# Optimization experiments

Hardware: AMD Instinct MI355X
Metric: run time of the kernel (lower is better)

Reference implementation:

```python
import jax, jax.numpy as jnp
import numpy as np

DIM = 256
HEADS = 4
B, N = 2, 4096
NEG = -1e9
EPS = 1e-5


def setup_inputs() -> dict:
    key = jax.random.key(0)
    ks = jax.random.split(key, 12)
    s = 0.02
    inp = {
        "x": jax.random.normal(ks[0], (B, N, DIM), dtype=jnp.float32),
        "adj": jax.random.randint(ks[1], (B, N, N), 0, 2, dtype=jnp.int32),
        "Wq": jax.random.normal(ks[2], (DIM, DIM), dtype=jnp.float32) * s,
        "bq": jnp.zeros((DIM,), jnp.float32),
        "Wk": jax.random.normal(ks[3], (DIM, DIM), dtype=jnp.float32) * s,
        "bk": jnp.zeros((DIM,), jnp.float32),
        "Wv": jax.random.normal(ks[4], (DIM, DIM), dtype=jnp.float32) * s,
        "bv": jnp.zeros((DIM,), jnp.float32),
        "Wo": jax.random.normal(ks[5], (DIM, DIM), dtype=jnp.float32) * s,
        "bo": jnp.zeros((DIM,), jnp.float32),
        "gamma": jnp.ones((DIM,), jnp.float32),
        "beta": jnp.zeros((DIM,), jnp.float32),
    }
    return inp


def reference(x, adj, Wq, bq, Wk, bk, Wv, bv, Wo, bo, gamma, beta):
    Bx, Nx, C = x.shape
    H = HEADS
    D = C // H
    scale = D ** (-0.5)
    # torch Linear: y = x @ W.T + b
    def proj(W, b):
        return (x @ W.T + b).reshape(Bx, Nx, H, D).transpose(0, 2, 1, 3)  # [B,H,N,D]
    q = proj(Wq, bq)
    k = proj(Wk, bk)
    v = proj(Wv, bv)
    attn = jnp.einsum("bhnd,bhmd->bhnm", q, k) * scale          # [B,H,N,N]
    attn = jnp.where(adj[:, None, :, :] == 0, NEG, attn)
    attn = jax.nn.softmax(attn, axis=-1)
    # dropout omitted (eval mode / deterministic reference)
    out = jnp.einsum("bhnm,bhmd->bhnd", attn, v)                # [B,H,N,D]
    out = out.transpose(0, 2, 1, 3).reshape(Bx, Nx, C)
    out = out @ Wo.T + bo
    mu = jnp.mean(out, axis=-1, keepdims=True)
    var = jnp.var(out, axis=-1, keepdims=True)
    return (out - mu) * jax.lax.rsqrt(var + EPS) * gamma + beta
```

## Files before the change

### kernel.cpp

```cpp
#include <hip/hip_runtime.h>
#include <stdint.h>

#define CDIM 256
#define HEADS 4
#define HD 64
#define NB 2
#define NN 4096

typedef unsigned short u16;
typedef unsigned char u8;
typedef unsigned long long u64;
typedef __attribute__((ext_vector_type(8))) short short8;
typedef __attribute__((ext_vector_type(4))) float f32x4;
typedef __attribute__((ext_vector_type(16))) float f32x16;

#define QSCALE 0.1803368801111244f

__device__ __forceinline__ u16 f2bf(float f) {
  union { float f; unsigned u; } v; v.f = f;
  return (u16)((v.u + 0x7fffu + ((v.u >> 16) & 1u)) >> 16);
}
__device__ __forceinline__ float bf2f(u16 u) {
  union { unsigned u; float f; } v; v.u = ((unsigned)u) << 16; return v.f;
}
__device__ __forceinline__ short8 fragf32(const float* p) {
  float4 a = reinterpret_cast<const float4*>(p)[0];
  float4 b = reinterpret_cast<const float4*>(p)[1];
  short8 h;
  h[0] = (short)f2bf(a.x); h[1] = (short)f2bf(a.y);
  h[2] = (short)f2bf(a.z); h[3] = (short)f2bf(a.w);
  h[4] = (short)f2bf(b.x); h[5] = (short)f2bf(b.y);
  h[6] = (short)f2bf(b.z); h[7] = (short)f2bf(b.w);
  return h;
}
__device__ __forceinline__ f32x16 zero16() {
  f32x16 z;
#pragma unroll
  for (int i = 0; i < 16; ++i) z[i] = 0.f;
  return z;
}
__device__ __forceinline__ unsigned cvt_pk_bf16(float lo, float hi) {
  unsigned r;
  asm("v_cvt_pk_bf16_f32 %0, %1, %2" : "=v"(r) : "v"(lo), "v"(hi));
  return r;
}
__device__ __forceinline__ void permlane32_swap(unsigned& a, unsigned& b) {
  asm("v_permlane32_swap_b32 %0, %1" : "+v"(a), "+v"(b));
}

__global__ __launch_bounds__(256) void prep(
    const int* __restrict__ adj, u8* __restrict__ bmb,
    const float* __restrict__ Wq, const float* __restrict__ Wk,
    const float* __restrict__ Wv, const float* __restrict__ Wo,
    u16* __restrict__ Wqb, u16* __restrict__ Wkb,
    u16* __restrict__ Wvb, u16* __restrict__ Wob) {
  const int blk = blockIdx.x;
  if (blk < 4096) {
    const int wave = threadIdx.x >> 6, lane = threadIdx.x & 63;
    const int c0 = blk * 16 + wave * 4;
#pragma unroll
    for (int it = 0; it < 4; ++it) {
      int c = c0 + it;
      int row = c >> 3, kb = (c & 7) * 512;
      const int* src = adj + (size_t)row * 4096 + kb + lane * 8;
      uint4 a = *reinterpret_cast<const uint4*>(src);
      uint4 b = *reinterpret_cast<const uint4*>(src + 4);
      unsigned byte = 0;
      byte |= (a.x != 0) ? 1u : 0u;
      byte |= (a.y != 0) ? 2u : 0u;
      byte |= (a.z != 0) ? 4u : 0u;
      byte |= (a.w != 0) ? 8u : 0u;
      byte |= (b.x != 0) ? 16u : 0u;
      byte |= (b.y != 0) ? 32u : 0u;
      byte |= (b.z != 0) ? 64u : 0u;
      byte |= (b.w != 0) ? 128u : 0u;
      bmb[(size_t)row * 512 + (c & 7) * 64 + lane] = (u8)byte;
    }
  } else {
    size_t base = ((size_t)(blk - 4096) * 256 + threadIdx.x) * 8;
    int w = (int)(base >> 16);
    size_t lo = base & 65535;
    const float* src;
    u16* dst;
    if (w == 0)      { src = Wq + lo; dst = Wqb + lo; }
    else if (w == 1) { src = Wk + lo; dst = Wkb + lo; }
    else if (w == 2) { src = Wv + lo; dst = Wvb + lo; }
    else             { src = Wo + lo; dst = Wob + lo; }
    *reinterpret_cast<short8*>(dst) = fragf32(src);
  }
}

__global__ __launch_bounds__(256) void qkv_gemm(
    const float* __restrict__ x,
    const u16* __restrict__ Wqb, const u16* __restrict__ Wkb,
    const u16* __restrict__ Wvb,
    const float* __restrict__ bq, const float* __restrict__ bk,
    const float* __restrict__ bv,
    u16* __restrict__ Qb, u16* __restrict__ Kb, u16* __restrict__ Vtb) {
  const int tid = threadIdx.x, w = tid >> 6, lane = tid & 63;
  const int quad = lane >> 4, l15 = lane & 15;
  const int tok0 = blockIdx.x * 16;
  const int b = tok0 >> 12, nl = tok0 & 4095;
  const int ym = blockIdx.y;

  f32x4 acc[4];
#pragma unroll
  for (int i = 0; i < 4; ++i) acc[i] = (f32x4){0.f, 0.f, 0.f, 0.f};

  if (ym < 2) {
    const u16* Wb = (ym == 0) ? Wqb : Wkb;
    const float* bias = (ym == 0) ? bq : bk;
    const float scale = (ym == 0) ? QSCALE : 1.0f;
    u16* outp = (ym == 0) ? Qb : Kb;
#pragma unroll
    for (int ks = 0; ks < 8; ++ks) {
      short8 af = fragf32(x + (size_t)(tok0 + l15) * 256 + ks * 32 + quad * 8);
#pragma unroll
      for (int ns = 0; ns < 4; ++ns) {
        short8 bf = *reinterpret_cast<const short8*>(
            &Wb[(size_t)(w * 64 + ns * 16 + l15) * 256 + ks * 32 + quad * 8]);
        acc[ns] = __builtin_amdgcn_mfma_f32_16x16x32_bf16(af, bf, acc[ns], 0, 0, 0);
      }
    }
#pragma unroll
    for (int ns = 0; ns < 4; ++ns) {
      int d = ns * 16 + l15;
      float bb = bias[w * 64 + d];
#pragma unroll
      for (int r = 0; r < 4; ++r) {
        int tok = nl + quad * 4 + r;
        outp[((size_t)(b * HEADS + w) * NN + tok) * HD + d] =
            f2bf((acc[ns][r] + bb) * scale);
      }
    }
  } else {
#pragma unroll
    for (int ks = 0; ks < 8; ++ks) {
      short8 xf = fragf32(x + (size_t)(tok0 + l15) * 256 + ks * 32 + quad * 8);
#pragma unroll
      for (int ms = 0; ms < 4; ++ms) {
        short8 wf = *reinterpret_cast<const short8*>(
            &Wvb[(size_t)(w * 64 + ms * 16 + l15) * 256 + ks * 32 + quad * 8]);
        acc[ms] = __builtin_amdgcn_mfma_f32_16x16x32_bf16(wf, xf, acc[ms], 0, 0, 0);
      }
    }
#pragma unroll
    for (int ms = 0; ms < 4; ++ms) {
#pragma unroll
      for (int r = 0; r < 4; ++r) {
        int d = ms * 16 + quad * 4 + r;
        float bb = bv[w * 64 + d];
        Vtb[((size_t)((b * HEADS + w) * HD + d)) * NN + nl + l15] =
            f2bf(acc[ms][r] + bb);
      }
    }
  }
}

__global__ __launch_bounds__(256, 3) void attn_mfma(
    const u16* __restrict__ Qb, const u16* __restrict__ Kb,
    const u16* __restrict__ Vtb, const u64* __restrict__ bm,
    u16* __restrict__ Opb, float* __restrict__ Lp) {
  __shared__ __align__(16) u16 KVs[2 * 8192];

  const int tid = threadIdx.x;
  const int wave = tid >> 6, lane = tid & 63;
  const int h5 = lane >> 5, l31 = lane & 31, l7 = lane & 7;
  const int bh = blockIdx.y, b = bh >> 2, h = bh & 3;
  const int q0 = blockIdx.x * 128 + wave * 32;
  const int quarter = blockIdx.z;
  const int key0 = quarter * 1024;
  const int NT = 16;

  const u16* qr = Qb + ((size_t)bh * NN + q0 + l31) * HD + h5 * 8;
  const short8 qf0 = *reinterpret_cast<const short8*>(qr);
  const short8 qf1 = *reinterpret_cast<const short8*>(qr + 16);
  const short8 qf2 = *reinterpret_cast<const short8*>(qr + 32);
  const short8 qf3 = *reinterpret_cast<const short8*>(qr + 48);

  short8 ones;
#pragma unroll
  for (int i = 0; i < 8; ++i) ones[i] = (short)0x3F80;

  f32x16 Oacc0 = zero16(), Oacc1 = zero16(), Oli = zero16();

  int sdk[4];
#pragma unroll
  for (int j = 0; j < 4; ++j) sdk[j] = ((2 * j + h5) ^ l7) << 3;

  const int srow = tid >> 2;
  const int wbu0 = ((((tid & 3) * 2)     ^ (srow & 7)) << 3) + srow * 64;
  const int wbu1 = ((((tid & 3) * 2 + 1) ^ (srow & 7)) << 3) + srow * 64;

  const u16* kbase = Kb + (size_t)bh * NN * HD + (size_t)key0 * HD;
  const u16* vbase = Vtb + (size_t)bh * HD * NN + key0;
  const u64* bmr = bm + ((size_t)b * NN + q0 + l31) * 64 + quarter * 16;

  uint4 k0, k1, v0, v1;
  {
    const uint4* kp = reinterpret_cast<const uint4*>(kbase) + tid * 2;
    k0 = kp[0]; k1 = kp[1];
    const u16* vp = vbase + (size_t)srow * NN + (tid & 3) * 16;
    v0 = *reinterpret_cast<const uint4*>(vp);
    v1 = *reinterpret_cast<const uint4*>(vp + 8);
  }
  *reinterpret_cast<uint4*>(&KVs[wbu0]) = k0;
  *reinterpret_cast<uint4*>(&KVs[wbu1]) = k1;
  *reinterpret_cast<uint4*>(&KVs[4096 + wbu0]) = v0;
  *reinterpret_cast<uint4*>(&KVs[4096 + wbu1]) = v1;
  {
    const uint4* kp = reinterpret_cast<const uint4*>(kbase + 4096) + tid * 2;
    k0 = kp[0]; k1 = kp[1];
    const u16* vp = vbase + (size_t)srow * NN + 64 + (tid & 3) * 16;
    v0 = *reinterpret_cast<const uint4*>(vp);
    v1 = *reinterpret_cast<const uint4*>(vp + 8);
  }
  u64 amc = bmr[0];

  for (int mt = 0; mt < NT; ++mt) {
    __syncthreads();
    const u64 am = amc;
    if (mt + 1 < NT) amc = bmr[mt + 1];
    const int cb = (mt & 1) * 8192;

    f32x16 s0 = zero16(), s1 = zero16();
    __builtin_amdgcn_s_setprio(1);
#pragma unroll
    for (int dk = 0; dk < 4; ++dk) {
      short8 a0 = *reinterpret_cast<const short8*>(&KVs[cb + l31 * 64 + sdk[dk]]);
      short8 a1 = *reinterpret_cast<const short8*>(&KVs[cb + 2048 + l31 * 64 + sdk[dk]]);
      const short8 qf = (dk == 0) ? qf0 : (dk == 1) ? qf1 : (dk == 2) ? qf2 : qf3;
      s0 = __builtin_amdgcn_mfma_f32_32x32x16_bf16(a0, qf, s0, 0, 0, 0);
      s1 = __builtin_amdgcn_mfma_f32_32x32x16_bf16(a1, qf, s1, 0, 0, 0);
    }
    __builtin_amdgcn_s_setprio(0);

    const u64 ash = am >> (4 * h5);
    const unsigned mlo = (unsigned)ash, mhi = (unsigned)(ash >> 32);

    uint4 pf0, pf1, pf2, pf3;
    {
      float pp[16];
#pragma unroll
      for (int r = 0; r < 16; ++r) {
        const int c = (r & 3) + 8 * (r >> 2);
        pp[r] = ((mlo >> c) & 1u) ? __builtin_amdgcn_exp2f(s0[r]) : 0.f;
      }
      unsigned wAe = cvt_pk_bf16(pp[0], pp[1]),  wBe = cvt_pk_bf16(pp[2], pp[3]);
      unsigned wAo = cvt_pk_bf16(pp[4], pp[5]),  wBo = cvt_pk_bf16(pp[6], pp[7]);
      permlane32_swap(wAe, wAo);
      permlane32_swap(wBe, wBo);
      pf0 = (uint4){wAe, wBe, wAo, wBo};
      wAe = cvt_pk_bf16(pp[8], pp[9]);   wBe = cvt_pk_bf16(pp[10], pp[11]);
      wAo = cvt_pk_bf16(pp[12], pp[13]); wBo = cvt_pk_bf16(pp[14], pp[15]);
      permlane32_swap(wAe, wAo);
      permlane32_swap(wBe, wBo);
      pf1 = (uint4){wAe, wBe, wAo, wBo};
    }
    {
      float pp[16];
#pragma unroll
      for (int r = 0; r < 16; ++r) {
        const int c = (r & 3) + 8 * (r >> 2);
        pp[r] = ((mhi >> c) & 1u) ? __builtin_amdgcn_exp2f(s1[r]) : 0.f;
      }
      unsigned wAe = cvt_pk_bf16(pp[0], pp[1]),  wBe = cvt_pk_bf16(pp[2], pp[3]);
      unsigned wAo = cvt_pk_bf16(pp[4], pp[5]),  wBo = cvt_pk_bf16(pp[6], pp[7]);
      permlane32_swap(wAe, wAo);
      permlane32_swap(wBe, wBo);
      pf2 = (uint4){wAe, wBe, wAo, wBo};
      wAe = cvt_pk_bf16(pp[8], pp[9]);   wBe = cvt_pk_bf16(pp[10], pp[11]);
      wAo = cvt_pk_bf16(pp[12], pp[13]); wBo = cvt_pk_bf16(pp[14], pp[15]);
      permlane32_swap(wAe, wAo);
      permlane32_swap(wBe, wBo);
      pf3 = (uint4){wAe, wBe, wAo, wBo};
    }

    __builtin_amdgcn_s_setprio(1);
#pragma unroll
    for (int kb = 0; kb < 4; ++kb) {
      union { uint4 u; short8 s; } cv;
      cv.u = (kb == 0) ? pf0 : (kb == 1) ? pf1 : (kb == 2) ? pf2 : pf3;
      const short8 pa = cv.s;
      Oli = __builtin_amdgcn_mfma_f32_32x32x16_bf16(pa, ones, Oli, 0, 0, 0);
      short8 vf0 = *reinterpret_cast<const short8*>(&KVs[cb + 4096 + l31 * 64 + sdk[kb]]);
      short8 vf1 = *reinterpret_cast<const short8*>(&KVs[cb + 6144 + l31 * 64 + sdk[kb]]);
      Oacc0 = __builtin_amdgcn_mfma_f32_32x32x16_bf16(pa, vf0, Oacc0, 0, 0, 0);
      Oacc1 = __builtin_amdgcn_mfma_f32_32x32x16_bf16(pa, vf1, Oacc1, 0, 0, 0);
    }
    __builtin_amdgcn_s_setprio(0);

    if (mt + 1 < NT) {
      const int nb = ((mt + 1) & 1) * 8192;
      *reinterpret_cast<uint4*>(&KVs[nb + wbu0]) = k0;
      *reinterpret_cast<uint4*>(&KVs[nb + wbu1]) = k1;
      *reinterpret_cast<uint4*>(&KVs[nb + 4096 + wbu0]) = v0;
      *reinterpret_cast<uint4*>(&KVs[nb + 4096 + wbu1]) = v1;
      if (mt + 2 < NT) {
        const uint4* kp =
            reinterpret_cast<const uint4*>(kbase + (size_t)(mt + 2) * 4096) + tid * 2;
        k0 = kp[0]; k1 = kp[1];
        const u16* vp = vbase + (size_t)srow * NN + (mt + 2) * 64 + (tid & 3) * 16;
        v0 = *reinterpret_cast<const uint4*>(vp);
        v1 = *reinterpret_cast<const uint4*>(vp + 8);
      }
    }
  }

  u16* ob = Opb + (size_t)(quarter * NB + b) * NN * CDIM;
#pragma unroll
  for (int r = 0; r < 16; ++r) {
    const int tok = q0 + (r & 3) + 8 * (r >> 2) + 4 * h5;
    u16* orow = ob + (size_t)tok * CDIM + h * HD;
    orow[l31] = f2bf(Oacc0[r]);
    orow[32 + l31] = f2bf(Oacc1[r]);
    if (l31 == 0) Lp[((size_t)quarter * 8 + bh) * NN + tok] = Oli[r];
  }
}

__global__ __launch_bounds__(256) void comb_oproj(
    const u16* __restrict__ Opb, const float* __restrict__ Lp,
    const u16* __restrict__ Wob, const float* __restrict__ bo,
    const float* __restrict__ gamma, const float* __restrict__ beta,
    float* __restrict__ out) {
  __shared__ u16 As[16 * 264];
  __shared__ float ys[16][264];
  __shared__ float linv[64];
  const int tid = threadIdx.x, w = tid >> 6, lane = tid & 63;
  const int quad = lane >> 4, l15 = lane & 15;
  const int tok0 = blockIdx.x * 16;
  const int b = tok0 >> 12, nl = tok0 & 4095;

  if (tid < 64) {
    int tokr = tid >> 2, hh = tid & 3;
    int bh = b * 4 + hh;
    int n = nl + tokr;
    float s = 0.f;
#pragma unroll
    for (int q = 0; q < 4; ++q)
      s += Lp[((size_t)q * 8 + bh) * NN + n];
    linv[tokr * 4 + hh] = (s > 0.f) ? (1.f / s) : 0.f;
  }
  __syncthreads();

  {
    int tokr = tid >> 4, ch0 = (tid & 15) * 16;
    size_t base = ((size_t)b * NN + nl + tokr) * CDIM + ch0;
    float inv = linv[tokr * 4 + (ch0 >> 6)];
    float acc16[16];
#pragma unroll
    for (int i = 0; i < 16; ++i) acc16[i] = 0.f;
#pragma unroll
    for (int q = 0; q < 4; ++q) {
      size_t qb = (size_t)q * 2097152 + base;
      uint4 a0 = *reinterpret_cast<const uint4*>(Opb + qb);
      uint4 a1 = *reinterpret_cast<const uint4*>(Opb + qb + 8);
      unsigned wa[8] = {a0.x, a0.y, a0.z, a0.w, a1.x, a1.y, a1.z, a1.w};
#pragma unroll
      for (int i = 0; i < 8; ++i) {
        acc16[2 * i]     += bf2f((u16)(wa[i] & 0xffffu));
        acc16[2 * i + 1] += bf2f((u16)(wa[i] >> 16));
      }
    }
    u16 ov[16];
#pragma unroll
    for (int i = 0; i < 16; ++i) ov[i] = f2bf(acc16[i] * inv);
    u16* dst = &As[tokr * 264 + ch0];
    *reinterpret_cast<uint4*>(dst) = *reinterpret_cast<uint4*>(ov);
    *reinterpret_cast<uint4*>(dst + 8) = *reinterpret_cast<uint4*>(ov + 8);
  }
  __syncthreads();

  f32x4 acc[4];
#pragma unroll
  for (int i = 0; i < 4; ++i) acc[i] = (f32x4){0.f, 0.f, 0.f, 0.f};
#pragma unroll
  for (int ks = 0; ks < 8; ++ks) {
    short8 af = *reinterpret_cast<const short8*>(&As[l15 * 264 + ks * 32 + quad * 8]);
#pragma unroll
    for (int ns = 0; ns < 4; ++ns) {
      short8 bf = *reinterpret_cast<const short8*>(
          &Wob[(size_t)(w * 64 + ns * 16 + l15) * 256 + ks * 32 + quad * 8]);
      acc[ns] = __builtin_amdgcn_mfma_f32_16x16x32_bf16(af, bf, acc[ns], 0, 0, 0);
    }
  }

#pragma unroll
  for (int ns = 0; ns < 4; ++ns) {
    int ch = w * 64 + ns * 16 + l15;
    float bb = bo[ch];
#pragma unroll
    for (int r = 0; r < 4; ++r) ys[quad * 4 + r][ch] = acc[ns][r] + bb;
  }
  __syncthreads();

  float g[4], bt[4];
#pragma unroll
  for (int i = 0; i < 4; ++i) {
    g[i] = gamma[lane + i * 64];
    bt[i] = beta[lane + i * 64];
  }
#pragma unroll
  for (int rr = 0; rr < 4; ++rr) {
    int r = w * 4 + rr;
    float v[4], s = 0.f, s2 = 0.f;
#pragma unroll
    for (int i = 0; i < 4; ++i) {
      v[i] = ys[r][lane + i * 64];
      s += v[i];
      s2 = fmaf(v[i], v[i], s2);
    }
#pragma unroll
    for (int off = 32; off > 0; off >>= 1) {
      s += __shfl_xor(s, off, 64);
      s2 += __shfl_xor(s2, off, 64);
    }
    float mu = s * (1.f / 256.f);
    float rs = rsqrtf(s2 * (1.f / 256.f) - mu * mu + 1e-5f);
    float* orow = out + (size_t)(tok0 + r) * 256;
#pragma unroll
    for (int i = 0; i < 4; ++i)
      orow[lane + i * 64] = (v[i] - mu) * rs * g[i] + bt[i];
  }
}

extern "C" void kernel_launch(void* const* d_in, const int* in_sizes, int n_in,
                              void* d_out, int out_size, void* d_ws, size_t ws_size,
                              hipStream_t stream) {
  const float* x     = (const float*)d_in[0];
  const int*   adj   = (const int*)d_in[1];
  const float* Wq    = (const float*)d_in[2];
  const float* bq    = (const float*)d_in[3];
  const float* Wk    = (const float*)d_in[4];
  const float* bk    = (const float*)d_in[5];
  const float* Wv    = (const float*)d_in[6];
  const float* bv    = (const float*)d_in[7];
  const float* Wo    = (const float*)d_in[8];
  const float* bo    = (const float*)d_in[9];
  const float* gamma = (const float*)d_in[10];
  const float* beta  = (const float*)d_in[11];
  float* out = (float*)d_out;

  const size_t PER = (size_t)NB * HEADS * NN * HD;
  u16* Wqb = (u16*)d_ws;
  u16* Wkb = Wqb + 65536;
  u16* Wvb = Wkb + 65536;
  u16* Wob = Wvb + 65536;
  u64* bmp = (u64*)(Wob + 65536);
  u16* Qb  = (u16*)(bmp + 524288);
  u16* Kb  = Qb + PER;
  u16* Vtb = Kb + PER;
  u16* Opb = Vtb + PER;
  float* Lp = (float*)(Opb + 4 * PER);

  const size_t NEED = (size_t)((u16*)(Lp + 131072) - (u16*)d_ws) * sizeof(u16);
  if (ws_size < NEED) return;

  prep<<<dim3(4224), dim3(256), 0, stream>>>(
      adj, (u8*)bmp, Wq, Wk, Wv, Wo, Wqb, Wkb, Wvb, Wob);

  qkv_gemm<<<dim3(512, 3), dim3(256), 0, stream>>>(
      x, Wqb, Wkb, Wvb, bq, bk, bv, Qb, Kb, Vtb);

  attn_mfma<<<dim3(NN / 128, NB * HEADS, 4), dim3(256), 0, stream>>>(
      Qb, Kb, Vtb, bmp, Opb, Lp);

  comb_oproj<<<dim3((NB * NN) / 16), dim3(256), 0, stream>>>(
      Opb, Lp, Wob, bo, gamma, beta, out);
}
```

Before: 309.9 us.

## Process two query tiles per wave and compute row sums with VALU

Each wave now handles 64 query rows (two 32-row tiles) instead of 32, so every K and V fragment read from shared memory feeds twice as many MFMAs. The softmax denominator is now accumulated with VALU adds plus a permlane swap instead of an extra MFMA against a ones vector. The grid is halved and launch bounds drop to two blocks per CU to make room for the doubled accumulators, which costs occupancy and latency hiding.

```diff
diff --git a/kernel.cpp b/kernel.cpp
--- a/kernel.cpp
+++ b/kernel.cpp
@@ -46,6 +46,30 @@
 }
 __device__ __forceinline__ void permlane32_swap(unsigned& a, unsigned& b) {
   asm("v_permlane32_swap_b32 %0, %1" : "+v"(a), "+v"(b));
+}
+__device__ __forceinline__ void smax_half(const f32x16& s, unsigned m32,
+                                          uint4& pfa, uint4& pfb, float& li) {
+  float pp[16];
+#pragma unroll
+  for (int r = 0; r < 16; ++r) {
+    const int c = (r & 3) + 8 * (r >> 2);
+    pp[r] = ((m32 >> c) & 1u) ? __builtin_amdgcn_exp2f(s[r]) : 0.f;
+  }
+  float t0 = (pp[0] + pp[1]) + (pp[2] + pp[3]);
+  float t1 = (pp[4] + pp[5]) + (pp[6] + pp[7]);
+  float t2 = (pp[8] + pp[9]) + (pp[10] + pp[11]);
+  float t3 = (pp[12] + pp[13]) + (pp[14] + pp[15]);
+  li += (t0 + t1) + (t2 + t3);
+  unsigned wAe = cvt_pk_bf16(pp[0], pp[1]),  wBe = cvt_pk_bf16(pp[2], pp[3]);
+  unsigned wAo = cvt_pk_bf16(pp[4], pp[5]),  wBo = cvt_pk_bf16(pp[6], pp[7]);
+  permlane32_swap(wAe, wAo);
+  permlane32_swap(wBe, wBo);
+  pfa = (uint4){wAe, wBe, wAo, wBo};
+  wAe = cvt_pk_bf16(pp[8], pp[9]);   wBe = cvt_pk_bf16(pp[10], pp[11]);
+  wAo = cvt_pk_bf16(pp[12], pp[13]); wBo = cvt_pk_bf16(pp[14], pp[15]);
+  permlane32_swap(wAe, wAo);
+  permlane32_swap(wBe, wBo);
+  pfb = (uint4){wAe, wBe, wAo, wBo};
 }
 
 __global__ __launch_bounds__(256) void prep(
@@ -157,7 +181,28 @@
   }
 }
 
-__global__ __launch_bounds__(256, 3) void attn_mfma(
+#define QKT_DK2(QFA, QFB, SD)                                                  \
+  { short8 ka_ = *reinterpret_cast<const short8*>(&KVs[cbq + l31 * 64 + SD]);  \
+    short8 kc_ =                                                               \
+        *reinterpret_cast<const short8*>(&KVs[cbq + 2048 + l31 * 64 + SD]);    \
+    sA0 = __builtin_amdgcn_mfma_f32_32x32x16_bf16(ka_, QFA, sA0, 0, 0, 0);     \
+    sB0 = __builtin_amdgcn_mfma_f32_32x32x16_bf16(ka_, QFB, sB0, 0, 0, 0);     \
+    sA1 = __builtin_amdgcn_mfma_f32_32x32x16_bf16(kc_, QFA, sA1, 0, 0, 0);     \
+    sB1 = __builtin_amdgcn_mfma_f32_32x32x16_bf16(kc_, QFB, sB1, 0, 0, 0); }
+
+#define PV_KB2(PFA, PFB, SD)                                                   \
+  { union { uint4 u; short8 s; } ua_, ub_;                                     \
+    ua_.u = PFA; ub_.u = PFB;                                                  \
+    short8 vf0_ =                                                              \
+        *reinterpret_cast<const short8*>(&KVs[cbq + 4096 + l31 * 64 + SD]);    \
+    short8 vf1_ =                                                              \
+        *reinterpret_cast<const short8*>(&KVs[cbq + 6144 + l31 * 64 + SD]);    \
+    OaccA0 = __builtin_amdgcn_mfma_f32_32x32x16_bf16(ua_.s, vf0_, OaccA0, 0, 0, 0); \
+    OaccA1 = __builtin_amdgcn_mfma_f32_32x32x16_bf16(ua_.s, vf1_, OaccA1, 0, 0, 0); \
+    OaccB0 = __builtin_amdgcn_mfma_f32_32x32x16_bf16(ub_.s, vf0_, OaccB0, 0, 0, 0); \
+    OaccB1 = __builtin_amdgcn_mfma_f32_32x32x16_bf16(ub_.s, vf1_, OaccB1, 0, 0, 0); }
+
+__global__ __launch_bounds__(256, 2) void attn_mfma(
     const u16* __restrict__ Qb, const u16* __restrict__ Kb,
     const u16* __restrict__ Vtb, const u64* __restrict__ bm,
     u16* __restrict__ Opb, float* __restrict__ Lp) {
@@ -167,22 +212,25 @@
   const int wave = tid >> 6, lane = tid & 63;
   const int h5 = lane >> 5, l31 = lane & 31, l7 = lane & 7;
   const int bh = blockIdx.y, b = bh >> 2, h = bh & 3;
-  const int q0 = blockIdx.x * 128 + wave * 32;
+  const int q0 = blockIdx.x * 256 + wave * 64;
   const int quarter = blockIdx.z;
   const int key0 = quarter * 1024;
   const int NT = 16;
 
-  const u16* qr = Qb + ((size_t)bh * NN + q0 + l31) * HD + h5 * 8;
-  const short8 qf0 = *reinterpret_cast<const short8*>(qr);
-  const short8 qf1 = *reinterpret_cast<const short8*>(qr + 16);
-  const short8 qf2 = *reinterpret_cast<const short8*>(qr + 32);
-  const short8 qf3 = *reinterpret_cast<const short8*>(qr + 48);
-
-  short8 ones;
-#pragma unroll
-  for (int i = 0; i < 8; ++i) ones[i] = (short)0x3F80;
-
-  f32x16 Oacc0 = zero16(), Oacc1 = zero16(), Oli = zero16();
+  const u16* qrA = Qb + ((size_t)bh * NN + q0 + l31) * HD + h5 * 8;
+  const short8 qfA0 = *reinterpret_cast<const short8*>(qrA);
+  const short8 qfA1 = *reinterpret_cast<const short8*>(qrA + 16);
+  const short8 qfA2 = *reinterpret_cast<const short8*>(qrA + 32);
+  const short8 qfA3 = *reinterpret_cast<const short8*>(qrA + 48);
+  const u16* qrB = qrA + 32 * HD;
+  const short8 qfB0 = *reinterpret_cast<const short8*>(qrB);
+  const short8 qfB1 = *reinterpret_cast<const short8*>(qrB + 16);
+  const short8 qfB2 = *reinterpret_cast<const short8*>(qrB + 32);
+  const short8 qfB3 = *reinterpret_cast<const short8*>(qrB + 48);
+
+  f32x16 OaccA0 = zero16(), OaccA1 = zero16();
+  f32x16 OaccB0 = zero16(), OaccB1 = zero16();
+  float liA = 0.f, liB = 0.f;
 
   int sdk[4];
 #pragma unroll
@@ -194,7 +242,8 @@
 
   const u16* kbase = Kb + (size_t)bh * NN * HD + (size_t)key0 * HD;
   const u16* vbase = Vtb + (size_t)bh * HD * NN + key0;
-  const u64* bmr = bm + ((size_t)b * NN + q0 + l31) * 64 + quarter * 16;
+  const u64* bmrA = bm + ((size_t)b * NN + q0 + l31) * 64 + quarter * 16;
+  const u64* bmrB = bmrA + (size_t)32 * 64;
 
   uint4 k0, k1, v0, v1;
   {
@@ -215,79 +264,37 @@
     v0 = *reinterpret_cast<const uint4*>(vp);
     v1 = *reinterpret_cast<const uint4*>(vp + 8);
   }
-  u64 amc = bmr[0];
+  u64 amA_c = bmrA[0], amB_c = bmrB[0];
 
   for (int mt = 0; mt < NT; ++mt) {
     __syncthreads();
-    const u64 am = amc;
-    if (mt + 1 < NT) amc = bmr[mt + 1];
-    const int cb = (mt & 1) * 8192;
-
-    f32x16 s0 = zero16(), s1 = zero16();
+    const u64 amA = amA_c, amB = amB_c;
+    if (mt + 1 < NT) { amA_c = bmrA[mt + 1]; amB_c = bmrB[mt + 1]; }
+    const int cbq = (mt & 1) * 8192;
+
+    f32x16 sA0 = zero16(), sA1 = zero16();
+    f32x16 sB0 = zero16(), sB1 = zero16();
     __builtin_amdgcn_s_setprio(1);
-#pragma unroll
-    for (int dk = 0; dk < 4; ++dk) {
-      short8 a0 = *reinterpret_cast<const short8*>(&KVs[cb + l31 * 64 + sdk[dk]]);
-      short8 a1 = *reinterpret_cast<const short8*>(&KVs[cb + 2048 + l31 * 64 + sdk[dk]]);
-      const short8 qf = (dk == 0) ? qf0 : (dk == 1) ? qf1 : (dk == 2) ? qf2 : qf3;
-      s0 = __builtin_amdgcn_mfma_f32_32x32x16_bf16(a0, qf, s0, 0, 0, 0);
-      s1 = __builtin_amdgcn_mfma_f32_32x32x16_bf16(a1, qf, s1, 0, 0, 0);
-    }
+    QKT_DK2(qfA0, qfB0, sdk[0]);
+    QKT_DK2(qfA1, qfB1, sdk[1]);
+    QKT_DK2(qfA2, qfB2, sdk[2]);
+    QKT_DK2(qfA3, qfB3, sdk[3]);
     __builtin_amdgcn_s_setprio(0);
 
-    const u64 ash = am >> (4 * h5);
-    const unsigned mlo = (unsigned)ash, mhi = (unsigned)(ash >> 32);
-
-    uint4 pf0, pf1, pf2, pf3;
-    {
-      float pp[16];
-#pragma unroll
-      for (int r = 0; r < 16; ++r) {
-        const int c = (r & 3) + 8 * (r >> 2);
-        pp[r] = ((mlo >> c) & 1u) ? __builtin_amdgcn_exp2f(s0[r]) : 0.f;
-      }
-      unsigned wAe = cvt_pk_bf16(pp[0], pp[1]),  wBe = cvt_pk_bf16(pp[2], pp[3]);
-      unsigned wAo = cvt_pk_bf16(pp[4], pp[5]),  wBo = cvt_pk_bf16(pp[6], pp[7]);
-      permlane32_swap(wAe, wAo);
-      permlane32_swap(wBe, wBo);
-      pf0 = (uint4){wAe, wBe, wAo, wBo};
-      wAe = cvt_pk_bf16(pp[8], pp[9]);   wBe = cvt_pk_bf16(pp[10], pp[11]);
-      wAo = cvt_pk_bf16(pp[12], pp[13]); wBo = cvt_pk_bf16(pp[14], pp[15]);
-      permlane32_swap(wAe, wAo);
-      permlane32_swap(wBe, wBo);
-      pf1 = (uint4){wAe, wBe, wAo, wBo};
-    }
-    {
-      float pp[16];
-#pragma unroll
-      for (int r = 0; r < 16; ++r) {
-        const int c = (r & 3) + 8 * (r >> 2);
-        pp[r] = ((mhi >> c) & 1u) ? __builtin_amdgcn_exp2f(s1[r]) : 0.f;
-      }
-      unsigned wAe = cvt_pk_bf16(pp[0], pp[1]),  wBe = cvt_pk_bf16(pp[2], pp[3]);
-      unsigned wAo = cvt_pk_bf16(pp[4], pp[5]),  wBo = cvt_pk_bf16(pp[6], pp[7]);
-      permlane32_swap(wAe, wAo);
-      permlane32_swap(wBe, wBo);
-      pf2 = (uint4){wAe, wBe, wAo, wBo};
-      wAe = cvt_pk_bf16(pp[8], pp[9]);   wBe = cvt_pk_bf16(pp[10], pp[11]);
-      wAo = cvt_pk_bf16(pp[12], pp[13]); wBo = cvt_pk_bf16(pp[14], pp[15]);
-      permlane32_swap(wAe, wAo);
-      permlane32_swap(wBe, wBo);
-      pf3 = (uint4){wAe, wBe, wAo, wBo};
-    }
+    const u64 ashA = amA >> (4 * h5);
+    const u64 ashB = amB >> (4 * h5);
+
+    uint4 pA0, pA1, pA2, pA3, pB0, pB1, pB2, pB3;
+    smax_half(sA0, (unsigned)ashA, pA0, pA1, liA);
+    smax_half(sA1, (unsigned)(ashA >> 32), pA2, pA3, liA);
+    smax_half(sB0, (unsigned)ashB, pB0, pB1, liB);
+    smax_half(sB1, (unsigned)(ashB >> 32), pB2, pB3, liB);
 
     __builtin_amdgcn_s_setprio(1);
-#pragma unroll
-    for (int kb = 0; kb < 4; ++kb) {
-      union { uint4 u; short8 s; } cv;
-      cv.u = (kb == 0) ? pf0 : (kb == 1) ? pf1 : (kb == 2) ? pf2 : pf3;
-      const short8 pa = cv.s;
-      Oli = __builtin_amdgcn_mfma_f32_32x32x16_bf16(pa, ones, Oli, 0, 0, 0);
-      short8 vf0 = *reinterpret_cast<const short8*>(&KVs[cb + 4096 + l31 * 64 + sdk[kb]]);
-      short8 vf1 = *reinterpret_cast<const short8*>(&KVs[cb + 6144 + l31 * 64 + sdk[kb]]);
-      Oacc0 = __builtin_amdgcn_mfma_f32_32x32x16_bf16(pa, vf0, Oacc0, 0, 0, 0);
-      Oacc1 = __builtin_amdgcn_mfma_f32_32x32x16_bf16(pa, vf1, Oacc1, 0, 0, 0);
-    }
+    PV_KB2(pA0, pB0, sdk[0]);
+    PV_KB2(pA1, pB1, sdk[1]);
+    PV_KB2(pA2, pB2, sdk[2]);
+    PV_KB2(pA3, pB3, sdk[3]);
     __builtin_amdgcn_s_setprio(0);
 
     if (mt + 1 < NT) {
@@ -310,11 +317,26 @@
   u16* ob = Opb + (size_t)(quarter * NB + b) * NN * CDIM;
 #pragma unroll
   for (int r = 0; r < 16; ++r) {
-    const int tok = q0 + (r & 3) + 8 * (r >> 2) + 4 * h5;
-    u16* orow = ob + (size_t)tok * CDIM + h * HD;
-    orow[l31] = f2bf(Oacc0[r]);
-    orow[32 + l31] = f2bf(Oacc1[r]);
-    if (l31 == 0) Lp[((size_t)quarter * 8 + bh) * NN + tok] = Oli[r];
+    const int tokA = q0 + (r & 3) + 8 * (r >> 2) + 4 * h5;
+    u16* orA = ob + (size_t)tokA * CDIM + h * HD;
+    orA[l31] = f2bf(OaccA0[r]);
+    orA[32 + l31] = f2bf(OaccA1[r]);
+    u16* orB = orA + (size_t)32 * CDIM;
+    orB[l31] = f2bf(OaccB0[r]);
+    orB[32 + l31] = f2bf(OaccB1[r]);
+  }
+  {
+    unsigned a0 = __float_as_uint(liA), a1 = a0;
+    permlane32_swap(a0, a1);
+    float liAf = __uint_as_float(a0) + __uint_as_float(a1);
+    unsigned b0 = __float_as_uint(liB), b1 = b0;
+    permlane32_swap(b0, b1);
+    float liBf = __uint_as_float(b0) + __uint_as_float(b1);
+    if (lane < 32) {
+      float* lrow = Lp + ((size_t)quarter * 8 + bh) * NN;
+      lrow[q0 + lane] = liAf;
+      lrow[q0 + 32 + lane] = liBf;
+    }
   }
 }
 
@@ -462,7 +484,7 @@
   qkv_gemm<<<dim3(512, 3), dim3(256), 0, stream>>>(
       x, Wqb, Wkb, Wvb, bq, bk, bv, Qb, Kb, Vtb);
 
-  attn_mfma<<<dim3(NN / 128, NB * HEADS, 4), dim3(256), 0, stream>>>(
+  attn_mfma<<<dim3(NN / 256, NB * HEADS, 4), dim3(256), 0, stream>>>(
       Qb, Kb, Vtb, bmp, Opb, Lp);
 
   comb_oproj<<<dim3((NB * NN) / 16), dim3(256), 0, stream>>>(
```

Result: no change. 307.6 us (-0.7%).
